# Optimization experiments

Hardware: AMD Instinct MI355X
Metric: run time of the kernel (lower is better)

The kernel has to match this reference:

```python
import jax, jax.numpy as jnp
import numpy as np

H = 16  # num_heads (matches init_kwargs)


def setup_inputs() -> dict:
    key = jax.random.key(0)
    ks = jax.random.split(key, 5)
    B, T, C = 4, 2048, 2048
    S = C // H
    g = 0.5 * (6.0 / (C + C)) ** 0.5 * (3.0 ** 0.5)  # ~xavier_uniform scale, gain 0.5
    x = jax.random.normal(ks[0], (B, T, C), dtype=jnp.float32)
    Wk = jax.random.uniform(ks[1], (C, C), jnp.float32, -g, g)
    Wv = jax.random.uniform(ks[2], (C, C), jnp.float32, -g, g)
    Wr = jax.random.uniform(ks[3], (C, C), jnp.float32, -g, g)
    Wo = jax.random.uniform(ks[4], (C, C), jnp.float32, -g, g)
    time_decay = jnp.full((H, S), -5.0, dtype=jnp.float32)
    time_first = jnp.zeros((H, S), dtype=jnp.float32)
    return {"x": x, "Wk": Wk, "Wv": Wv, "Wr": Wr, "Wo": Wo,
            "time_decay": time_decay, "time_first": time_first}


def _wkv(k, v, time_decay, time_first):
    # k, v: [B, T, H, S] float32
    decay = jnp.exp(-jnp.exp(time_decay.astype(jnp.float32)))  # [H, S]
    first = jnp.exp(time_first.astype(jnp.float32))            # [H, S]
    w = jnp.exp(jnp.clip(k.astype(jnp.float32), -10.0, 10.0))  # [B, T, H, S]
    # t==0 branch (state = first*w0*v0) == uniform recurrence with w0 scaled by first
    w = w.at[:, 0].multiply(first)
    wt = jnp.swapaxes(w, 0, 1)                    # [T, B, H, S]
    vt = jnp.swapaxes(v.astype(jnp.float32), 0, 1)

    def step(carry, inp):
        num, den = carry
        w_t, v_t = inp
        num = decay * num + w_t * v_t
        den = decay * den + w_t
        return (num, den), num / (den + 1e-6)

    B, _, _, S = k.shape
    init = (jnp.zeros((B, H, S), jnp.float32), jnp.zeros((B, H, S), jnp.float32))
    _, wkv = jax.lax.scan(step, init, (wt, vt))   # [T, B, H, S]
    return jnp.swapaxes(wkv, 0, 1).astype(k.dtype)  # [B, T, H, S]


def reference(x, Wk, Wv, Wr, Wo, time_decay, time_first):
    B, T, C = x.shape
    S = C // H
    k = (x @ Wk.T).reshape(B, T, H, S)
    v = (x @ Wv.T).reshape(B, T, H, S)
    r = (x @ Wr.T).reshape(B, T, H, S)
    wkv = _wkv(k, v, time_decay, time_first)
    rwkv = (jax.nn.sigmoid(r) * wkv).reshape(B, T, C)
    return rwkv @ Wo.T
```

## Files before the change

### kernel.cpp

```cpp
#include <hip/hip_runtime.h>
#include <hip/hip_bf16.h>

using bf16 = __hip_bfloat16;
using floatx4 = __attribute__((ext_vector_type(4))) float;
using bf16x8  = __attribute__((ext_vector_type(8))) __bf16;
using bf16x2  = __attribute__((ext_vector_type(2))) __bf16;

#define MDIM 8192
#define NDIM 2048
#define KDIM 2048
#define TSEQ 2048
#define BB   4
#define CDIM 2048
#define NCHUNK 64
#define TCHUNK 32

typedef __attribute__((address_space(1))) void gvoid_t;
typedef __attribute__((address_space(3))) void lvoid_t;

__device__ __forceinline__ void load_lds16(const void* g, void* l) {
  __builtin_amdgcn_global_load_lds((gvoid_t*)(void*)g, (lvoid_t*)l, 16, 0, 0);
}

__global__ __launch_bounds__(256) void cvt_x(const float* __restrict__ s,
                                             __bf16* __restrict__ d) {
  const int i = (blockIdx.x * 256 + threadIdx.x) * 8;
  float4 a = *(const float4*)(s + i);
  float4 b = *(const float4*)(s + i + 4);
  bf16x8 o;
  o[0] = (__bf16)a.x; o[1] = (__bf16)a.y; o[2] = (__bf16)a.z; o[3] = (__bf16)a.w;
  o[4] = (__bf16)b.x; o[5] = (__bf16)b.y; o[6] = (__bf16)b.z; o[7] = (__bf16)b.w;
  *(bf16x8*)(d + i) = o;
}

__global__ __launch_bounds__(256) void cvt_w(const float* __restrict__ s0,
                                             const float* __restrict__ s1,
                                             const float* __restrict__ s2,
                                             const float* __restrict__ s3,
                                             __bf16* __restrict__ d0,
                                             __bf16* __restrict__ d1,
                                             __bf16* __restrict__ d2,
                                             __bf16* __restrict__ d3) {
  const float* s = (blockIdx.y == 0) ? s0 : (blockIdx.y == 1) ? s1
                 : (blockIdx.y == 2) ? s2 : s3;
  __bf16*      d = (blockIdx.y == 0) ? d0 : (blockIdx.y == 1) ? d1
                 : (blockIdx.y == 2) ? d2 : d3;
  const int i = (blockIdx.x * 256 + threadIdx.x) * 8;
  float4 a = *(const float4*)(s + i);
  float4 b = *(const float4*)(s + i + 4);
  bf16x8 o;
  o[0] = (__bf16)a.x; o[1] = (__bf16)a.y; o[2] = (__bf16)a.z; o[3] = (__bf16)a.w;
  o[4] = (__bf16)b.x; o[5] = (__bf16)b.y; o[6] = (__bf16)b.z; o[7] = (__bf16)b.w;
  *(bf16x8*)(d + i) = o;
}

template <typename CT>
__device__ __forceinline__ void gemm_body(const __bf16* __restrict__ A,
                                          const __bf16* __restrict__ B,
                                          CT* __restrict__ C) {
  __shared__ __bf16 sA[128 * 32];
  __shared__ __bf16 sB[128 * 32];
  const int tid  = threadIdx.x;
  const int lane = tid & 63;
  const int wave = tid >> 6;
  const int wm = (wave >> 1) * 64;
  const int wn = (wave & 1) * 64;
  const int bm = blockIdx.x, bn = blockIdx.y;

  floatx4 acc[4][4] = {};

  const int srow  = tid >> 2;
  const int shalf = (tid & 3) ^ ((tid >> 3) & 3);
  const __bf16* Ag = A + (size_t)(bm * 128 + srow) * KDIM + shalf * 8;
  const __bf16* Bg = B + (size_t)(bn * 128 + srow) * KDIM + shalf * 8;
  __bf16* sAp = sA + tid * 8;
  __bf16* sBp = sB + tid * 8;

  const int fr  = lane & 15;
  const int fk4 = lane >> 4;
  int chA[4], chB[4];
#pragma unroll
  for (int i = 0; i < 4; ++i) {
    const int ra = wm + i * 16 + fr;
    const int rb = wn + i * 16 + fr;
    chA[i] = (ra << 2) | (fk4 ^ ((ra >> 1) & 3));
    chB[i] = (rb << 2) | (fk4 ^ ((rb >> 1) & 3));
  }

  for (int kt = 0; kt < KDIM; kt += 32) {
    load_lds16(Ag,                      sAp);
    load_lds16(Ag + (size_t)64 * KDIM,  sAp + 2048);
    load_lds16(Bg,                      sBp);
    load_lds16(Bg + (size_t)64 * KDIM,  sBp + 2048);
    Ag += 32; Bg += 32;
    __syncthreads();

    bf16x8 af[4], bfr[4];
#pragma unroll
    for (int i = 0; i < 4; ++i)
      af[i] = *(const bf16x8*)(sA + chA[i] * 8);
#pragma unroll
    for (int j = 0; j < 4; ++j)
      bfr[j] = *(const bf16x8*)(sB + chB[j] * 8);
#pragma unroll
    for (int i = 0; i < 4; ++i)
#pragma unroll
      for (int j = 0; j < 4; ++j)
        acc[i][j] = __builtin_amdgcn_mfma_f32_16x16x32_bf16(af[i], bfr[j], acc[i][j], 0, 0, 0);
    __syncthreads();
  }

  const int crow = (lane >> 4) * 4;
  const int ccol = lane & 15;
#pragma unroll
  for (int i = 0; i < 4; ++i)
#pragma unroll
    for (int j = 0; j < 4; ++j) {
      const size_t r0 = (size_t)(bm * 128 + wm + i * 16 + crow);
      const int    c0 = bn * 128 + wn + j * 16 + ccol;
#pragma unroll
      for (int rg = 0; rg < 4; ++rg)
        C[(r0 + rg) * NDIM + c0] = (CT)(acc[i][j][rg]);
    }
}

__global__ __launch_bounds__(256) void gemm_qkv(const __bf16* __restrict__ x,
                                                const __bf16* __restrict__ Wk,
                                                const __bf16* __restrict__ Wv,
                                                const __bf16* __restrict__ Wr,
                                                __bf16* __restrict__ kb,
                                                __bf16* __restrict__ vb,
                                                __bf16* __restrict__ rb) {
  const __bf16* Bsel = (blockIdx.z == 0) ? Wk : (blockIdx.z == 1) ? Wv : Wr;
  __bf16*       Csel = (blockIdx.z == 0) ? kb : (blockIdx.z == 1) ? vb : rb;
  gemm_body<__bf16>(x, Bsel, Csel);
}

__global__ __launch_bounds__(256) void gemm_o(const __bf16* __restrict__ A,
                                              const __bf16* __restrict__ B,
                                              float* __restrict__ C) {
  gemm_body<float>(A, B, C);
}

__global__ __launch_bounds__(256) void wkv_summary(
    const __bf16* __restrict__ kb, const __bf16* __restrict__ vb,
    const float* __restrict__ td, const float* __restrict__ tf,
    float* __restrict__ nsum, float* __restrict__ dsum) {
  const int c0 = (blockIdx.x * 256 + threadIdx.x) * 2;
  const int chunk = blockIdx.y;
  const int b = blockIdx.z;
  const float dc0 = __expf(-__expf(td[c0]));
  const float dc1 = __expf(-__expf(td[c0 + 1]));
  const float fi0 = __expf(tf[c0]);
  const float fi1 = __expf(tf[c0 + 1]);
  size_t base = ((size_t)b * TSEQ + (size_t)chunk * TCHUNK) * CDIM + c0;
  float n0 = 0.f, d0 = 0.f, n1 = 0.f, d1 = 0.f;
#pragma unroll 4
  for (int t = 0; t < TCHUNK; ++t) {
    bf16x2 k2 = *(const bf16x2*)(kb + base + (size_t)t * CDIM);
    bf16x2 v2 = *(const bf16x2*)(vb + base + (size_t)t * CDIM);
    float k0f = fminf(fmaxf((float)k2[0], -10.f), 10.f);
    float k1f = fminf(fmaxf((float)k2[1], -10.f), 10.f);
    float w0 = __expf(k0f), w1 = __expf(k1f);
    if (chunk == 0 && t == 0) { w0 *= fi0; w1 *= fi1; }
    n0 = dc0 * n0 + w0 * (float)v2[0];
    d0 = dc0 * d0 + w0;
    n1 = dc1 * n1 + w1 * (float)v2[1];
    d1 = dc1 * d1 + w1;
  }
  const size_t si = (size_t)(chunk * BB + b) * CDIM + c0;
  *(float2*)(nsum + si) = make_float2(n0, n1);
  *(float2*)(dsum + si) = make_float2(d0, d1);
}

__global__ __launch_bounds__(256) void wkv_apply(
    const __bf16* __restrict__ kb, const __bf16* __restrict__ vb,
    __bf16* __restrict__ rb,
    const float* __restrict__ td, const float* __restrict__ tf,
    const float* __restrict__ nsum, const float* __restrict__ dsum) {
  const int c0 = (blockIdx.x * 256 + threadIdx.x) * 2;
  const int chunk = blockIdx.y;
  const int b = blockIdx.z;
  const float ed0 = __expf(td[c0]);
  const float ed1 = __expf(td[c0 + 1]);
  const float dc0 = __expf(-ed0);
  const float dc1 = __expf(-ed1);
  const float dT0 = __expf(-ed0 * (float)TCHUNK);
  const float dT1 = __expf(-ed1 * (float)TCHUNK);
  const float fi0 = __expf(tf[c0]);
  const float fi1 = __expf(tf[c0 + 1]);

  float n0 = 0.f, d0 = 0.f, n1 = 0.f, d1 = 0.f;
  for (int j = 0; j < chunk; ++j) {
    const size_t si = (size_t)(j * BB + b) * CDIM + c0;
    float2 ns = *(const float2*)(nsum + si);
    float2 ds = *(const float2*)(dsum + si);
    n0 = dT0 * n0 + ns.x;  d0 = dT0 * d0 + ds.x;
    n1 = dT1 * n1 + ns.y;  d1 = dT1 * d1 + ds.y;
  }
  size_t base = ((size_t)b * TSEQ + (size_t)chunk * TCHUNK) * CDIM + c0;
#pragma unroll 2
  for (int t = 0; t < TCHUNK; ++t) {
    const size_t idx = base + (size_t)t * CDIM;
    bf16x2 k2 = *(const bf16x2*)(kb + idx);
    bf16x2 v2 = *(const bf16x2*)(vb + idx);
    bf16x2 r2 = *(const bf16x2*)(rb + idx);
    float k0f = fminf(fmaxf((float)k2[0], -10.f), 10.f);
    float k1f = fminf(fmaxf((float)k2[1], -10.f), 10.f);
    float w0 = __expf(k0f), w1 = __expf(k1f);
    if (chunk == 0 && t == 0) { w0 *= fi0; w1 *= fi1; }
    n0 = dc0 * n0 + w0 * (float)v2[0];
    d0 = dc0 * d0 + w0;
    n1 = dc1 * n1 + w1 * (float)v2[1];
    d1 = dc1 * d1 + w1;
    const float wkv0 = n0 * __builtin_amdgcn_rcpf(d0 + 1e-6f);
    const float wkv1 = n1 * __builtin_amdgcn_rcpf(d1 + 1e-6f);
    const float sr0 = __builtin_amdgcn_rcpf(1.f + __expf(-(float)r2[0]));
    const float sr1 = __builtin_amdgcn_rcpf(1.f + __expf(-(float)r2[1]));
    bf16x2 o;
    o[0] = (__bf16)(sr0 * wkv0);
    o[1] = (__bf16)(sr1 * wkv1);
    *(bf16x2*)(rb + idx) = o;
  }
}

extern "C" void kernel_launch(void* const* d_in, const int* in_sizes, int n_in,
                              void* d_out, int out_size, void* d_ws, size_t ws_size,
                              hipStream_t stream) {
  const float* x  = (const float*)d_in[0];
  const float* Wk = (const float*)d_in[1];
  const float* Wv = (const float*)d_in[2];
  const float* Wr = (const float*)d_in[3];
  const float* Wo = (const float*)d_in[4];
  const float* td = (const float*)d_in[5];
  const float* tf = (const float*)d_in[6];
  float* out = (float*)d_out;

  char* ws = (char*)d_ws;
  const size_t matX = (size_t)MDIM * KDIM * sizeof(__bf16);
  const size_t matW = (size_t)NDIM * KDIM * sizeof(__bf16);
  __bf16* xb  = (__bf16*)(ws);
  __bf16* wkb = (__bf16*)(ws + matX);
  __bf16* wvb = (__bf16*)(ws + matX + matW);
  __bf16* wrb = (__bf16*)(ws + matX + 2 * matW);
  __bf16* wob = (__bf16*)(ws + matX + 3 * matW);
  __bf16* kb  = (__bf16*)(ws + matX + 4 * matW);
  __bf16* vb  = (__bf16*)(ws + 2 * matX + 4 * matW);
  __bf16* rb  = (__bf16*)(ws + 3 * matX + 4 * matW);
  float* nsum = (float*)(ws + 4 * matX + 4 * matW);
  float* dsum = nsum + (size_t)NCHUNK * BB * CDIM;

  dim3 blk(256);
  cvt_x<<<dim3(MDIM * KDIM / (8 * 256)), blk, 0, stream>>>(x, xb);
  cvt_w<<<dim3(NDIM * KDIM / (8 * 256), 4), blk, 0, stream>>>(
      Wk, Wv, Wr, Wo, wkb, wvb, wrb, wob);

  dim3 gq(MDIM / 128, NDIM / 128, 3);
  gemm_qkv<<<gq, blk, 0, stream>>>(xb, wkb, wvb, wrb, kb, vb, rb);
  dim3 gw(CDIM / 512, NCHUNK, BB);
  wkv_summary<<<gw, blk, 0, stream>>>(kb, vb, td, tf, nsum, dsum);
  wkv_apply<<<gw, blk, 0, stream>>>(kb, vb, rb, td, tf, nsum, dsum);
  dim3 go(MDIM / 128, NDIM / 128, 1);
  gemm_o<<<go, blk, 0, stream>>>(rb, wob, out);
}
```

Baseline: 528.7 us.

## Merge conversion kernels, add chunk-prefix scan kernel, set GEMM occupancy hints

Folds the x and weight fp32-to-bf16 conversions into one launch. Adds a separate wkv_scan kernel that turns per-chunk summaries into exclusive prefix states in place, so each wkv_apply block reads one prefix instead of looping over all earlier chunks (quadratic to linear carry work). Adds a min-blocks-per-CU hint of 4 to both GEMMs, which may cap registers and risk spills. The scan adds one extra launch and a serial loop over 64 chunks running on only 16 blocks.

Measured after the change: 526.8 us. No clear change (-0.4%).

```diff
diff --git a/kernel.cpp b/kernel.cpp
--- a/kernel.cpp
+++ b/kernel.cpp
@@ -22,29 +22,22 @@
   __builtin_amdgcn_global_load_lds((gvoid_t*)(void*)g, (lvoid_t*)l, 16, 0, 0);
 }
 
-__global__ __launch_bounds__(256) void cvt_x(const float* __restrict__ s,
-                                             __bf16* __restrict__ d) {
-  const int i = (blockIdx.x * 256 + threadIdx.x) * 8;
-  float4 a = *(const float4*)(s + i);
-  float4 b = *(const float4*)(s + i + 4);
-  bf16x8 o;
-  o[0] = (__bf16)a.x; o[1] = (__bf16)a.y; o[2] = (__bf16)a.z; o[3] = (__bf16)a.w;
-  o[4] = (__bf16)b.x; o[5] = (__bf16)b.y; o[6] = (__bf16)b.z; o[7] = (__bf16)b.w;
-  *(bf16x8*)(d + i) = o;
-}
-
-__global__ __launch_bounds__(256) void cvt_w(const float* __restrict__ s0,
-                                             const float* __restrict__ s1,
-                                             const float* __restrict__ s2,
-                                             const float* __restrict__ s3,
-                                             __bf16* __restrict__ d0,
-                                             __bf16* __restrict__ d1,
-                                             __bf16* __restrict__ d2,
-                                             __bf16* __restrict__ d3) {
-  const float* s = (blockIdx.y == 0) ? s0 : (blockIdx.y == 1) ? s1
-                 : (blockIdx.y == 2) ? s2 : s3;
-  __bf16*      d = (blockIdx.y == 0) ? d0 : (blockIdx.y == 1) ? d1
-                 : (blockIdx.y == 2) ? d2 : d3;
+__global__ __launch_bounds__(256) void cvt_all(
+    const float* __restrict__ x,
+    const float* __restrict__ Wk, const float* __restrict__ Wv,
+    const float* __restrict__ Wr, const float* __restrict__ Wo,
+    __bf16* __restrict__ xb,
+    __bf16* __restrict__ wkb, __bf16* __restrict__ wvb,
+    __bf16* __restrict__ wrb, __bf16* __restrict__ wob) {
+  const size_t WN = (size_t)NDIM * KDIM;
+  const int slice = blockIdx.y;
+  const float* s;
+  __bf16* d;
+  if (slice < 4) { s = x + (size_t)slice * WN; d = xb + (size_t)slice * WN; }
+  else {
+    s = (slice == 4) ? Wk : (slice == 5) ? Wv : (slice == 6) ? Wr : Wo;
+    d = (slice == 4) ? wkb : (slice == 5) ? wvb : (slice == 6) ? wrb : wob;
+  }
   const int i = (blockIdx.x * 256 + threadIdx.x) * 8;
   float4 a = *(const float4*)(s + i);
   float4 b = *(const float4*)(s + i + 4);
@@ -124,21 +117,21 @@
     }
 }
 
-__global__ __launch_bounds__(256) void gemm_qkv(const __bf16* __restrict__ x,
-                                                const __bf16* __restrict__ Wk,
-                                                const __bf16* __restrict__ Wv,
-                                                const __bf16* __restrict__ Wr,
-                                                __bf16* __restrict__ kb,
-                                                __bf16* __restrict__ vb,
-                                                __bf16* __restrict__ rb) {
+__global__ __launch_bounds__(256, 4) void gemm_qkv(const __bf16* __restrict__ x,
+                                                   const __bf16* __restrict__ Wk,
+                                                   const __bf16* __restrict__ Wv,
+                                                   const __bf16* __restrict__ Wr,
+                                                   __bf16* __restrict__ kb,
+                                                   __bf16* __restrict__ vb,
+                                                   __bf16* __restrict__ rb) {
   const __bf16* Bsel = (blockIdx.z == 0) ? Wk : (blockIdx.z == 1) ? Wv : Wr;
   __bf16*       Csel = (blockIdx.z == 0) ? kb : (blockIdx.z == 1) ? vb : rb;
   gemm_body<__bf16>(x, Bsel, Csel);
 }
 
-__global__ __launch_bounds__(256) void gemm_o(const __bf16* __restrict__ A,
-                                              const __bf16* __restrict__ B,
-                                              float* __restrict__ C) {
+__global__ __launch_bounds__(256, 4) void gemm_o(const __bf16* __restrict__ A,
+                                                 const __bf16* __restrict__ B,
+                                                 float* __restrict__ C) {
   gemm_body<float>(A, B, C);
 }
 
@@ -173,6 +166,25 @@
   *(float2*)(dsum + si) = make_float2(d0, d1);
 }
 
+__global__ __launch_bounds__(256) void wkv_scan(
+    const float* __restrict__ td,
+    float* __restrict__ nsum, float* __restrict__ dsum) {
+  const int c0 = (blockIdx.x * 256 + threadIdx.x) * 2;
+  const int b = blockIdx.y;
+  const float dT0 = __expf(-__expf(td[c0]) * (float)TCHUNK);
+  const float dT1 = __expf(-__expf(td[c0 + 1]) * (float)TCHUNK);
+  float pn0 = 0.f, pd0 = 0.f, pn1 = 0.f, pd1 = 0.f;
+  for (int j = 0; j < NCHUNK; ++j) {
+    const size_t si = (size_t)(j * BB + b) * CDIM + c0;
+    float2 Sn = *(const float2*)(nsum + si);
+    float2 Sd = *(const float2*)(dsum + si);
+    *(float2*)(nsum + si) = make_float2(pn0, pn1);
+    *(float2*)(dsum + si) = make_float2(pd0, pd1);
+    pn0 = dT0 * pn0 + Sn.x;  pn1 = dT1 * pn1 + Sn.y;
+    pd0 = dT0 * pd0 + Sd.x;  pd1 = dT1 * pd1 + Sd.y;
+  }
+}
+
 __global__ __launch_bounds__(256) void wkv_apply(
     const __bf16* __restrict__ kb, const __bf16* __restrict__ vb,
     __bf16* __restrict__ rb,
@@ -181,23 +193,16 @@
   const int c0 = (blockIdx.x * 256 + threadIdx.x) * 2;
   const int chunk = blockIdx.y;
   const int b = blockIdx.z;
-  const float ed0 = __expf(td[c0]);
-  const float ed1 = __expf(td[c0 + 1]);
-  const float dc0 = __expf(-ed0);
-  const float dc1 = __expf(-ed1);
-  const float dT0 = __expf(-ed0 * (float)TCHUNK);
-  const float dT1 = __expf(-ed1 * (float)TCHUNK);
+  const float dc0 = __expf(-__expf(td[c0]));
+  const float dc1 = __expf(-__expf(td[c0 + 1]));
   const float fi0 = __expf(tf[c0]);
   const float fi1 = __expf(tf[c0 + 1]);
 
-  float n0 = 0.f, d0 = 0.f, n1 = 0.f, d1 = 0.f;
-  for (int j = 0; j < chunk; ++j) {
-    const size_t si = (size_t)(j * BB + b) * CDIM + c0;
-    float2 ns = *(const float2*)(nsum + si);
-    float2 ds = *(const float2*)(dsum + si);
-    n0 = dT0 * n0 + ns.x;  d0 = dT0 * d0 + ds.x;
-    n1 = dT1 * n1 + ns.y;  d1 = dT1 * d1 + ds.y;
-  }
+  const size_t si = (size_t)(chunk * BB + b) * CDIM + c0;
+  float2 pn = *(const float2*)(nsum + si);
+  float2 pd = *(const float2*)(dsum + si);
+  float n0 = pn.x, n1 = pn.y, d0 = pd.x, d1 = pd.y;
+
   size_t base = ((size_t)b * TSEQ + (size_t)chunk * TCHUNK) * CDIM + c0;
 #pragma unroll 2
   for (int t = 0; t < TCHUNK; ++t) {
@@ -251,14 +256,14 @@
   float* dsum = nsum + (size_t)NCHUNK * BB * CDIM;
 
   dim3 blk(256);
-  cvt_x<<<dim3(MDIM * KDIM / (8 * 256)), blk, 0, stream>>>(x, xb);
-  cvt_w<<<dim3(NDIM * KDIM / (8 * 256), 4), blk, 0, stream>>>(
-      Wk, Wv, Wr, Wo, wkb, wvb, wrb, wob);
+  cvt_all<<<dim3(NDIM * KDIM / (8 * 256), 8), blk, 0, stream>>>(
+      x, Wk, Wv, Wr, Wo, xb, wkb, wvb, wrb, wob);
 
   dim3 gq(MDIM / 128, NDIM / 128, 3);
   gemm_qkv<<<gq, blk, 0, stream>>>(xb, wkb, wvb, wrb, kb, vb, rb);
   dim3 gw(CDIM / 512, NCHUNK, BB);
   wkv_summary<<<gw, blk, 0, stream>>>(kb, vb, td, tf, nsum, dsum);
+  wkv_scan<<<dim3(CDIM / 512, BB), blk, 0, stream>>>(td, nsum, dsum);
   wkv_apply<<<gw, blk, 0, stream>>>(kb, vb, rb, td, tf, nsum, dsum);
   dim3 go(MDIM / 128, NDIM / 128, 1);
   gemm_o<<<go, blk, 0, stream>>>(rb, wob, out);
```
